# Kernel optimization log

Measured on AMD Instinct MI355X. Metric: run time of the kernel, lower is better.

Reference implementation:

```python
import jax, jax.numpy as jnp
import numpy as np


def setup_inputs() -> dict:
    key = jax.random.key(0)
    x = jax.random.normal(key, (8192, 4096), dtype=jnp.float32)
    return {"x": x}


def reference(x) -> jnp.ndarray:
    # Sparsemax along the last axis (dim=-1), matching the torch module's math.
    n = x.shape[-1]
    x = x - jnp.max(x, axis=-1, keepdims=True)
    # sort descending
    zs = jnp.flip(jnp.sort(x, axis=-1), axis=-1)  # [B, N]
    r = jnp.arange(1, n + 1, dtype=x.dtype)       # [N]
    bound = 1.0 + r * zs
    cum_zs = jnp.cumsum(zs, axis=-1)
    is_gt = (bound > cum_zs).astype(x.dtype)
    k = jnp.max(is_gt * r, axis=-1, keepdims=True)          # support size
    taus = (jnp.sum(is_gt * zs, axis=-1, keepdims=True) - 1.0) / k
    return jnp.maximum(jnp.zeros_like(x), x - taus)
```

## Files before the change

### kernel.cpp

```cpp
#include <hip/hip_runtime.h>


#define COLS 4096
#define WAVES_PER_BLOCK 4
#define CAND_CAP 960
#define MAX_ITERS 32

__global__ __launch_bounds__(256) void sparsemax_kernel(
    const float* __restrict__ x, float* __restrict__ out, int rows) {
  __shared__ __align__(16) float rowbuf[WAVES_PER_BLOCK][COLS];
  __shared__ __align__(16) float cand[WAVES_PER_BLOCK][CAND_CAP];
  __shared__ int cnt[WAVES_PER_BLOCK];

  const int lane = threadIdx.x & 63;
  const int wid = threadIdx.x >> 6;
  const long row = (long)blockIdx.x * WAVES_PER_BLOCK + wid;
  if (row >= rows) return;

  if (lane == 0) cnt[wid] = 0;

  const float4* __restrict__ xr =
      reinterpret_cast<const float4*>(x + row * COLS);
  float4* __restrict__ outr = reinterpret_cast<float4*>(out + row * COLS);
  float4* rb = reinterpret_cast<float4*>(rowbuf[wid]);

  float m = -INFINITY;
#pragma unroll
  for (int j = 0; j < 16; ++j) {
    float4 v = xr[lane + j * 64];
    rb[lane + j * 64] = v;
    m = fmaxf(m, fmaxf(fmaxf(v.x, v.y), fmaxf(v.z, v.w)));
  }
#pragma unroll
  for (int off = 32; off > 0; off >>= 1) m = fmaxf(m, __shfl_xor(m, off));

  const float thr = m - 1.0f;

#pragma unroll
  for (int j = 0; j < 16; ++j) {
    float4 v = rb[lane + j * 64];
    if (v.x > thr) { int p = atomicAdd(&cnt[wid], 1); if (p < CAND_CAP) cand[wid][p] = v.x; }
    if (v.y > thr) { int p = atomicAdd(&cnt[wid], 1); if (p < CAND_CAP) cand[wid][p] = v.y; }
    if (v.z > thr) { int p = atomicAdd(&cnt[wid], 1); if (p < CAND_CAP) cand[wid][p] = v.z; }
    if (v.w > thr) { int p = atomicAdd(&cnt[wid], 1); if (p < CAND_CAP) cand[wid][p] = v.w; }
  }

  const int nc = cnt[wid];
  float tau = thr;

  if (nc <= CAND_CAP) {
    for (int it = 0; it < MAX_ITERS; ++it) {
      float s = 0.0f;
      int c = 0;
      for (int k = lane; k < nc; k += 64) {
        float v = cand[wid][k];
        if (v > tau) { s += v; c += 1; }
      }
#pragma unroll
      for (int off = 32; off > 0; off >>= 1) {
        s += __shfl_xor(s, off);
        c += __shfl_xor(c, off);
      }
      float ntau = (s - 1.0f) / (float)c;
      if (ntau == tau) break;
      tau = ntau;
    }
  } else {
    for (int it = 0; it < MAX_ITERS; ++it) {
      float s = 0.0f;
      int c = 0;
#pragma unroll
      for (int j = 0; j < 16; ++j) {
        float4 v = rb[lane + j * 64];
        if (v.x > tau) { s += v.x; c += 1; }
        if (v.y > tau) { s += v.y; c += 1; }
        if (v.z > tau) { s += v.z; c += 1; }
        if (v.w > tau) { s += v.w; c += 1; }
      }
#pragma unroll
      for (int off = 32; off > 0; off >>= 1) {
        s += __shfl_xor(s, off);
        c += __shfl_xor(c, off);
      }
      float ntau = (s - 1.0f) / (float)c;
      if (ntau == tau) break;
      tau = ntau;
    }
  }

#pragma unroll
  for (int j = 0; j < 16; ++j) {
    float4 v = rb[lane + j * 64];
    float4 o;
    o.x = fmaxf(v.x - tau, 0.0f);
    o.y = fmaxf(v.y - tau, 0.0f);
    o.z = fmaxf(v.z - tau, 0.0f);
    o.w = fmaxf(v.w - tau, 0.0f);
    outr[lane + j * 64] = o;
  }
}

extern "C" void kernel_launch(void* const* d_in, const int* in_sizes, int n_in,
                              void* d_out, int out_size, void* d_ws,
                              size_t ws_size, hipStream_t stream) {
  const float* x = (const float*)d_in[0];
  float* out = (float*)d_out;
  const int rows = in_sizes[0] / COLS;
  const int blocks = (rows + WAVES_PER_BLOCK - 1) / WAVES_PER_BLOCK;
  sparsemax_kernel<<<blocks, 256, 0, stream>>>(x, out, rows);
}
```

Baseline: 232.6 us.

## Process one row per block in registers instead of per-wave LDS row buffers

Switches from one row per wave (staging the full 16KB row in shared memory) to one row per 256-thread block. Each thread holds its 16 values in registers, and max, candidate count and sums are combined across waves through small shared arrays and barriers. Removing the 64KB+ per-block LDS row buffer is meant to raise occupancy and drop the LDS round trips. Output is written with nontemporal stores. The cost is extra block-level barriers and one shared atomic counter contended by all 256 threads.

```diff
diff --git a/kernel.cpp b/kernel.cpp
--- a/kernel.cpp
+++ b/kernel.cpp
@@ -2,59 +2,70 @@
 
 
 #define COLS 4096
-#define WAVES_PER_BLOCK 4
-#define CAND_CAP 960
+#define THREADS 256
+#define NW 4
+#define CAND_CAP 1024
 #define MAX_ITERS 32
 
-__global__ __launch_bounds__(256) void sparsemax_kernel(
-    const float* __restrict__ x, float* __restrict__ out, int rows) {
-  __shared__ __align__(16) float rowbuf[WAVES_PER_BLOCK][COLS];
-  __shared__ __align__(16) float cand[WAVES_PER_BLOCK][CAND_CAP];
-  __shared__ int cnt[WAVES_PER_BLOCK];
+typedef float f32x4 __attribute__((ext_vector_type(4)));
 
-  const int lane = threadIdx.x & 63;
-  const int wid = threadIdx.x >> 6;
-  const long row = (long)blockIdx.x * WAVES_PER_BLOCK + wid;
-  if (row >= rows) return;
+__global__ __launch_bounds__(THREADS) void sparsemax_kernel(
+    const float* __restrict__ x, float* __restrict__ out) {
+  __shared__ float cand[CAND_CAP];
+  __shared__ float wmax[NW];
+  __shared__ float wsum[NW];
+  __shared__ int wcnt[NW];
+  __shared__ int cnt;
 
-  if (lane == 0) cnt[wid] = 0;
+  const int tid = threadIdx.x;
+  const int lane = tid & 63;
+  const int wid = tid >> 6;
+  const long row = blockIdx.x;
 
-  const float4* __restrict__ xr =
-      reinterpret_cast<const float4*>(x + row * COLS);
-  float4* __restrict__ outr = reinterpret_cast<float4*>(out + row * COLS);
-  float4* rb = reinterpret_cast<float4*>(rowbuf[wid]);
+  const f32x4* __restrict__ xr =
+      reinterpret_cast<const f32x4*>(x + row * COLS);
+  f32x4* __restrict__ outr = reinterpret_cast<f32x4*>(out + row * COLS);
 
-  float m = -INFINITY;
-#pragma unroll
-  for (int j = 0; j < 16; ++j) {
-    float4 v = xr[lane + j * 64];
-    rb[lane + j * 64] = v;
-    m = fmaxf(m, fmaxf(fmaxf(v.x, v.y), fmaxf(v.z, v.w)));
-  }
+  if (tid == 0) cnt = 0;
+
+  f32x4 v0 = xr[tid];
+  f32x4 v1 = xr[tid + THREADS];
+  f32x4 v2 = xr[tid + 2 * THREADS];
+  f32x4 v3 = xr[tid + 3 * THREADS];
+
+  float m = fmaxf(fmaxf(v0.x, v0.y), fmaxf(v0.z, v0.w));
+  m = fmaxf(m, fmaxf(fmaxf(v1.x, v1.y), fmaxf(v1.z, v1.w)));
+  m = fmaxf(m, fmaxf(fmaxf(v2.x, v2.y), fmaxf(v2.z, v2.w)));
+  m = fmaxf(m, fmaxf(fmaxf(v3.x, v3.y), fmaxf(v3.z, v3.w)));
 #pragma unroll
   for (int off = 32; off > 0; off >>= 1) m = fmaxf(m, __shfl_xor(m, off));
+  if (lane == 0) wmax[wid] = m;
+  __syncthreads();
+  m = fmaxf(fmaxf(wmax[0], wmax[1]), fmaxf(wmax[2], wmax[3]));
 
   const float thr = m - 1.0f;
 
-#pragma unroll
-  for (int j = 0; j < 16; ++j) {
-    float4 v = rb[lane + j * 64];
-    if (v.x > thr) { int p = atomicAdd(&cnt[wid], 1); if (p < CAND_CAP) cand[wid][p] = v.x; }
-    if (v.y > thr) { int p = atomicAdd(&cnt[wid], 1); if (p < CAND_CAP) cand[wid][p] = v.y; }
-    if (v.z > thr) { int p = atomicAdd(&cnt[wid], 1); if (p < CAND_CAP) cand[wid][p] = v.z; }
-    if (v.w > thr) { int p = atomicAdd(&cnt[wid], 1); if (p < CAND_CAP) cand[wid][p] = v.w; }
+#define EMIT(val)                                   \
+  if ((val) > thr) {                                \
+    int p = atomicAdd(&cnt, 1);                     \
+    if (p < CAND_CAP) cand[p] = (val);              \
   }
+  EMIT(v0.x) EMIT(v0.y) EMIT(v0.z) EMIT(v0.w)
+  EMIT(v1.x) EMIT(v1.y) EMIT(v1.z) EMIT(v1.w)
+  EMIT(v2.x) EMIT(v2.y) EMIT(v2.z) EMIT(v2.w)
+  EMIT(v3.x) EMIT(v3.y) EMIT(v3.z) EMIT(v3.w)
+#undef EMIT
+  __syncthreads();
+  const int nc = cnt;
 
-  const int nc = cnt[wid];
   float tau = thr;
-
   if (nc <= CAND_CAP) {
     for (int it = 0; it < MAX_ITERS; ++it) {
       float s = 0.0f;
       int c = 0;
       for (int k = lane; k < nc; k += 64) {
-        float v = cand[wid][k];
-        if (v > tau) { s += v; c += 1; }
+        float q = cand[k];
+        if (q > tau) { s += q; c += 1; }
       }
 #pragma unroll
       for (int off = 32; off > 0; off >>= 1) {
@@ -69,35 +80,42 @@
     for (int it = 0; it < MAX_ITERS; ++it) {
       float s = 0.0f;
       int c = 0;
-#pragma unroll
-      for (int j = 0; j < 16; ++j) {
-        float4 v = rb[lane + j * 64];
-        if (v.x > tau) { s += v.x; c += 1; }
-        if (v.y > tau) { s += v.y; c += 1; }
-        if (v.z > tau) { s += v.z; c += 1; }
-        if (v.w > tau) { s += v.w; c += 1; }
-      }
+#define ACC(val)                      \
+  if ((val) > tau) { s += (val); c += 1; }
+      ACC(v0.x) ACC(v0.y) ACC(v0.z) ACC(v0.w)
+      ACC(v1.x) ACC(v1.y) ACC(v1.z) ACC(v1.w)
+      ACC(v2.x) ACC(v2.y) ACC(v2.z) ACC(v2.w)
+      ACC(v3.x) ACC(v3.y) ACC(v3.z) ACC(v3.w)
+#undef ACC
 #pragma unroll
       for (int off = 32; off > 0; off >>= 1) {
         s += __shfl_xor(s, off);
         c += __shfl_xor(c, off);
       }
+      if (lane == 0) { wsum[wid] = s; wcnt[wid] = c; }
+      __syncthreads();
+      s = wsum[0] + wsum[1] + wsum[2] + wsum[3];
+      c = wcnt[0] + wcnt[1] + wcnt[2] + wcnt[3];
       float ntau = (s - 1.0f) / (float)c;
+      __syncthreads();
       if (ntau == tau) break;
       tau = ntau;
     }
   }
 
-#pragma unroll
-  for (int j = 0; j < 16; ++j) {
-    float4 v = rb[lane + j * 64];
-    float4 o;
-    o.x = fmaxf(v.x - tau, 0.0f);
-    o.y = fmaxf(v.y - tau, 0.0f);
-    o.z = fmaxf(v.z - tau, 0.0f);
-    o.w = fmaxf(v.w - tau, 0.0f);
-    outr[lane + j * 64] = o;
-  }
+  f32x4 o;
+  o.x = fmaxf(v0.x - tau, 0.0f); o.y = fmaxf(v0.y - tau, 0.0f);
+  o.z = fmaxf(v0.z - tau, 0.0f); o.w = fmaxf(v0.w - tau, 0.0f);
+  __builtin_nontemporal_store(o, outr + tid);
+  o.x = fmaxf(v1.x - tau, 0.0f); o.y = fmaxf(v1.y - tau, 0.0f);
+  o.z = fmaxf(v1.z - tau, 0.0f); o.w = fmaxf(v1.w - tau, 0.0f);
+  __builtin_nontemporal_store(o, outr + tid + THREADS);
+  o.x = fmaxf(v2.x - tau, 0.0f); o.y = fmaxf(v2.y - tau, 0.0f);
+  o.z = fmaxf(v2.z - tau, 0.0f); o.w = fmaxf(v2.w - tau, 0.0f);
+  __builtin_nontemporal_store(o, outr + tid + 2 * THREADS);
+  o.x = fmaxf(v3.x - tau, 0.0f); o.y = fmaxf(v3.y - tau, 0.0f);
+  o.z = fmaxf(v3.z - tau, 0.0f); o.w = fmaxf(v3.w - tau, 0.0f);
+  __builtin_nontemporal_store(o, outr + tid + 3 * THREADS);
 }
 
 extern "C" void kernel_launch(void* const* d_in, const int* in_sizes, int n_in,
@@ -106,6 +124,5 @@
   const float* x = (const float*)d_in[0];
   float* out = (float*)d_out;
   const int rows = in_sizes[0] / COLS;
-  const int blocks = (rows + WAVES_PER_BLOCK - 1) / WAVES_PER_BLOCK;
-  sparsemax_kernel<<<blocks, 256, 0, stream>>>(x, out, rows);
+  sparsemax_kernel<<<rows, THREADS, 0, stream>>>(x, out);
 }
```

Measured after the change: 231.3 us. Within noise of the previous version (-0.5%).
